# Kernel optimization log

Measured on AMD Instinct MI355X. Metric: run time of the kernel, lower is better.

The kernel has to match this reference:

```python
import jax, jax.numpy as jnp
import numpy as np

B, N, DIN, DOUT, L = 32, 512, 768, 256, 512
NEG = -9.0e15
SLOPE = 0.2  # LeakyReLU negative slope


def setup_inputs() -> dict:
    key = jax.random.key(0)
    ks = jax.random.split(key, 7)
    h = jax.random.normal(ks[0], (B, N, DIN), dtype=jnp.float32)
    adj = jax.random.randint(ks[1], (B, N, N), 0, 2, dtype=jnp.int32)
    positions = jax.random.randint(ks[2], (B, N), 0, L, dtype=jnp.int32)
    W = jax.random.normal(ks[3], (DIN, DOUT), dtype=jnp.float32) * 0.02
    a1 = jax.random.normal(ks[4], (DOUT,), dtype=jnp.float32) * 0.02
    a2 = jax.random.normal(ks[5], (DOUT,), dtype=jnp.float32) * 0.02
    pos_table = jax.random.normal(ks[6], (L, DOUT), dtype=jnp.float32) * 0.02
    return {"h": h, "adj": adj, "positions": positions, "W": W,
            "a1": a1, "a2": a2, "pos_table": pos_table}


def reference(h, adj, positions, W, a1, a2, pos_table):
    # Wh = W(h) + pos_emb(positions)   -> [B, N, DOUT]
    Wh = jnp.einsum('bnd,de->bne', h, W) + pos_table[positions]
    # Pairwise GAT score: e_ij = leakyrelu(a1 . Wh_i + a2 . Wh_j)
    # (identical math to concat([Wh_i, Wh_j]) @ [a1; a2], without the O(N^2*2D) tensor)
    s1 = jnp.einsum('bnd,d->bn', Wh, a1)  # source term   [B, N]
    s2 = jnp.einsum('bnd,d->bn', Wh, a2)  # target term   [B, N]
    e = jax.nn.leaky_relu(s1[:, :, None] + s2[:, None, :], negative_slope=SLOPE)  # [B,N,N]
    # adjacency mask + softmax over neighbors (dropout is identity in eval)
    attention = jax.nn.softmax(jnp.where(adj > 0, e, NEG), axis=-1)  # [B, N, N]
    h_prime = jnp.einsum('bij,bjd->bid', attention, Wh)  # [B, N, DOUT]
    return h_prime, attention
```

## Files before the change

### kernel.cpp

```cpp
#include <hip/hip_runtime.h>
#include <math.h>

#define B 32
#define N 512
#define DIN 768
#define DOUT 256
#define NEGV -9.0e15f
#define SLOPE 0.2f

typedef __bf16 bf16x8 __attribute__((ext_vector_type(8)));
typedef float f32x4 __attribute__((ext_vector_type(4)));
typedef unsigned short us8 __attribute__((ext_vector_type(8)));

__device__ __forceinline__ unsigned short f2b(float f) {
    union { float f; unsigned u; } v; v.f = f;
    unsigned r = v.u + 0x7FFF + ((v.u >> 16) & 1);
    return (unsigned short)(r >> 16);
}

__device__ __forceinline__ float b2f(unsigned short h) {
    union { unsigned u; float f; } v; v.u = ((unsigned)h) << 16;
    return v.f;
}

__device__ __forceinline__ void gload_lds16(const unsigned short* g, unsigned short* l) {
    __builtin_amdgcn_global_load_lds(
        (const __attribute__((address_space(1))) unsigned int*)(unsigned long long)(uintptr_t)g,
        (__attribute__((address_space(3))) unsigned int*)(uintptr_t)l,
        16, 0, 0);
}

__global__ __launch_bounds__(256) void conv_h(const float4* __restrict__ in,
                                              ushort4* __restrict__ out) {
    int idx = blockIdx.x * 256 + threadIdx.x;
    float4 v = in[idx];
    ushort4 o;
    o.x = f2b(v.x); o.y = f2b(v.y); o.z = f2b(v.z); o.w = f2b(v.w);
    out[idx] = o;
}

__global__ __launch_bounds__(256) void conv_wt(const float* __restrict__ W,
                                               unsigned short* __restrict__ WT) {
    __shared__ unsigned short tile[64][65];
    const int k0 = blockIdx.x * 64, n0 = blockIdx.y * 64;
    const int t = threadIdx.x;
    const int cl = t & 63, cg = t >> 6;
#pragma unroll
    for (int i = 0; i < 16; ++i) {
        int k = cg * 16 + i;
        tile[cl][k] = f2b(W[(size_t)(k0 + k) * DOUT + n0 + cl]);
    }
    __syncthreads();
#pragma unroll
    for (int i = 0; i < 16; ++i) {
        int n = cg * 16 + i;
        WT[(size_t)(n0 + n) * DIN + k0 + cl] = tile[n][cl];
    }
}

__global__ __launch_bounds__(256) void wh_mfma(
    const unsigned short* __restrict__ hA,
    const unsigned short* __restrict__ WT,
    const int*   __restrict__ pos,
    const float* __restrict__ ptab,
    unsigned short* __restrict__ WhT)
{
    constexpr int K = DIN;
    __shared__ unsigned short As[128 * 32];
    __shared__ unsigned short Bs[64 * 32];
    __shared__ unsigned short tileT[64 * 136];

    const int t    = threadIdx.x;
    const int lane = t & 63;
    const int w    = t >> 6;
    const int m0   = blockIdx.y * 128;
    const int n0   = blockIdx.x * 64;

    const int ar0 = t >> 2,          aq0 = (t & 3) ^ ((ar0 >> 1) & 3);
    const int ar1 = (256 + t) >> 2,  aq1 = (t & 3) ^ ((ar1 >> 1) & 3);
    const int br  = t >> 2,          bq  = (t & 3) ^ ((br >> 1) & 3);
    const unsigned short* gA0 = hA + (size_t)(m0 + ar0) * K + aq0 * 8;
    const unsigned short* gA1 = hA + (size_t)(m0 + ar1) * K + aq1 * 8;
    const unsigned short* gB  = WT + (size_t)(n0 + br) * K + bq * 8;
    unsigned short* lA0 = As + (t & 192) * 8;
    unsigned short* lA1 = As + 2048 + (t & 192) * 8;
    unsigned short* lB  = Bs + (t & 192) * 8;

    const int wm = (w & 1) * 64, wn = (w >> 1) * 32;
    const int l15 = lane & 15, q = lane >> 4;
    int aoff[4], boff[2];
#pragma unroll
    for (int i = 0; i < 4; ++i) {
        int rm = wm + i * 16 + l15;
        aoff[i] = (rm * 4 + (q ^ ((rm >> 1) & 3))) * 8;
    }
#pragma unroll
    for (int i = 0; i < 2; ++i) {
        int rn = wn + i * 16 + l15;
        boff[i] = (rn * 4 + (q ^ ((rn >> 1) & 3))) * 8;
    }

    f32x4 acc[4][2];
#pragma unroll
    for (int i = 0; i < 4; ++i)
#pragma unroll
        for (int j = 0; j < 2; ++j) acc[i][j] = (f32x4){0.f, 0.f, 0.f, 0.f};

    for (int k0 = 0; k0 < K; k0 += 32) {
        gload_lds16(gA0 + k0, lA0);
        gload_lds16(gA1 + k0, lA1);
        gload_lds16(gB + k0, lB);
        __syncthreads();
        bf16x8 af[4], bfr[2];
#pragma unroll
        for (int i = 0; i < 4; ++i) af[i] = *(const bf16x8*)(As + aoff[i]);
#pragma unroll
        for (int i = 0; i < 2; ++i) bfr[i] = *(const bf16x8*)(Bs + boff[i]);
#pragma unroll
        for (int mi = 0; mi < 4; ++mi)
#pragma unroll
            for (int ni = 0; ni < 2; ++ni)
                acc[mi][ni] = __builtin_amdgcn_mfma_f32_16x16x32_bf16(
                    af[mi], bfr[ni], acc[mi][ni], 0, 0, 0);
        __syncthreads();
    }

#pragma unroll
    for (int mi = 0; mi < 4; ++mi) {
        const int jb = wm + mi * 16 + q * 4;
#pragma unroll
        for (int ni = 0; ni < 2; ++ni) {
            const int nl = wn + ni * 16 + l15;
            ushort4 pk;
            unsigned short* pp = (unsigned short*)&pk;
#pragma unroll
            for (int r = 0; r < 4; ++r) {
                int m = m0 + jb + r;
                int p = pos[m];
                pp[r] = f2b(acc[mi][ni][r] + ptab[(size_t)p * DOUT + n0 + nl]);
            }
            *(ushort4*)&tileT[nl * 136 + jb] = pk;
        }
    }
    __syncthreads();
    const int bb = m0 >> 9, j0 = m0 & 511;
#pragma unroll
    for (int rr = 0; rr < 4; ++rr) {
        int nl = (t >> 4) + rr * 16;
        int jl = (t & 15) * 8;
        us8 v = *(const us8*)&tileT[nl * 136 + jl];
        *(us8*)&WhT[((size_t)bb * DOUT + n0 + nl) * N + j0 + jl] = v;
    }
}

__global__ __launch_bounds__(256) void rowdots(
    const unsigned short* __restrict__ WhT,
    const float* __restrict__ a1, const float* __restrict__ a2,
    float* __restrict__ s1, float* __restrict__ s2)
{
    const int b = blockIdx.x >> 3, jc = blockIdx.x & 7;
    const int jl = threadIdx.x & 63, dq = threadIdx.x >> 6;
    const int j = jc * 64 + jl;
    const unsigned short* base = WhT + (size_t)b * DOUT * N + j;
    float v1 = 0.f, v2 = 0.f;
#pragma unroll 8
    for (int dd = 0; dd < 64; ++dd) {
        int d = dq * 64 + dd;
        float wv = b2f(base[(size_t)d * N]);
        v1 += wv * a1[d];
        v2 += wv * a2[d];
    }
    __shared__ float r1[4][64], r2[4][64];
    r1[dq][jl] = v1; r2[dq][jl] = v2;
    __syncthreads();
    if (dq == 0) {
        s1[b * N + j] = r1[0][jl] + r1[1][jl] + r1[2][jl] + r1[3][jl];
        s2[b * N + j] = r2[0][jl] + r2[1][jl] + r2[2][jl] + r2[3][jl];
    }
}

__global__ __launch_bounds__(256) void attn_softmax(
    const float* __restrict__ s1,
    const float* __restrict__ s2,
    const int*   __restrict__ adj,
    float*       __restrict__ att,
    unsigned short* __restrict__ attb)
{
    const int row = blockIdx.x;
    const int b   = row >> 9;
    const int t   = threadIdx.x;

    const float s1i = s1[row];
    float vals[2];
#pragma unroll
    for (int c = 0; c < 2; ++c) {
        int j = t + c * 256;
        float v = s1i + s2[b * N + j];
        v = v > 0.0f ? v : SLOPE * v;
        vals[c] = (adj[(size_t)row * N + j] > 0) ? v : NEGV;
    }

    __shared__ float red[4];
    __shared__ float bcast;

    float m = fmaxf(vals[0], vals[1]);
#pragma unroll
    for (int off = 32; off > 0; off >>= 1)
        m = fmaxf(m, __shfl_down(m, off));
    const int wid = t >> 6;
    if ((t & 63) == 0) red[wid] = m;
    __syncthreads();
    if (t == 0) bcast = fmaxf(fmaxf(red[0], red[1]), fmaxf(red[2], red[3]));
    __syncthreads();
    m = bcast;

    float p0 = __expf(vals[0] - m);
    float p1 = __expf(vals[1] - m);
    float s = p0 + p1;
#pragma unroll
    for (int off = 32; off > 0; off >>= 1)
        s += __shfl_down(s, off);
    __syncthreads();
    if ((t & 63) == 0) red[wid] = s;
    __syncthreads();
    if (t == 0) bcast = red[0] + red[1] + red[2] + red[3];
    __syncthreads();
    const float inv = 1.0f / bcast;

    float o0 = p0 * inv, o1 = p1 * inv;
    att[(size_t)row * N + t]        = o0;
    att[(size_t)row * N + t + 256]  = o1;
    attb[(size_t)row * N + t]       = f2b(o0);
    attb[(size_t)row * N + t + 256] = f2b(o1);
}

__global__ __launch_bounds__(256) void hp_mfma(
    const unsigned short* __restrict__ attb,
    const unsigned short* __restrict__ WhT,
    float* __restrict__ hp)
{
    constexpr int K = N;
    __shared__ unsigned short As[128 * 32];
    __shared__ unsigned short Bs[64 * 32];

    const int t    = threadIdx.x;
    const int lane = t & 63;
    const int w    = t >> 6;
    const int bb   = blockIdx.z;
    const int m0   = blockIdx.y * 128;
    const int n0   = blockIdx.x * 64;

    const unsigned short* A  = attb + (size_t)bb * N * N;
    const unsigned short* Bg = WhT  + (size_t)bb * DOUT * N;

    const int ar0 = t >> 2,          aq0 = (t & 3) ^ ((ar0 >> 1) & 3);
    const int ar1 = (256 + t) >> 2,  aq1 = (t & 3) ^ ((ar1 >> 1) & 3);
    const int br  = t >> 2,          bq  = (t & 3) ^ ((br >> 1) & 3);
    const unsigned short* gA0 = A  + (size_t)(m0 + ar0) * K + aq0 * 8;
    const unsigned short* gA1 = A  + (size_t)(m0 + ar1) * K + aq1 * 8;
    const unsigned short* gB  = Bg + (size_t)(n0 + br) * K + bq * 8;
    unsigned short* lA0 = As + (t & 192) * 8;
    unsigned short* lA1 = As + 2048 + (t & 192) * 8;
    unsigned short* lB  = Bs + (t & 192) * 8;

    const int wm = (w & 1) * 64, wn = (w >> 1) * 32;
    const int l15 = lane & 15, q = lane >> 4;
    int aoff[4], boff[2];
#pragma unroll
    for (int i = 0; i < 4; ++i) {
        int rm = wm + i * 16 + l15;
        aoff[i] = (rm * 4 + (q ^ ((rm >> 1) & 3))) * 8;
    }
#pragma unroll
    for (int i = 0; i < 2; ++i) {
        int rn = wn + i * 16 + l15;
        boff[i] = (rn * 4 + (q ^ ((rn >> 1) & 3))) * 8;
    }

    f32x4 acc[4][2];
#pragma unroll
    for (int i = 0; i < 4; ++i)
#pragma unroll
        for (int j = 0; j < 2; ++j) acc[i][j] = (f32x4){0.f, 0.f, 0.f, 0.f};

    for (int k0 = 0; k0 < K; k0 += 32) {
        gload_lds16(gA0 + k0, lA0);
        gload_lds16(gA1 + k0, lA1);
        gload_lds16(gB + k0, lB);
        __syncthreads();
        bf16x8 af[4], bfr[2];
#pragma unroll
        for (int i = 0; i < 4; ++i) af[i] = *(const bf16x8*)(As + aoff[i]);
#pragma unroll
        for (int i = 0; i < 2; ++i) bfr[i] = *(const bf16x8*)(Bs + boff[i]);
#pragma unroll
        for (int mi = 0; mi < 4; ++mi)
#pragma unroll
            for (int ni = 0; ni < 2; ++ni)
                acc[mi][ni] = __builtin_amdgcn_mfma_f32_16x16x32_bf16(
                    af[mi], bfr[ni], acc[mi][ni], 0, 0, 0);
        __syncthreads();
    }

#pragma unroll
    for (int mi = 0; mi < 4; ++mi) {
#pragma unroll
        for (int r = 0; r < 4; ++r) {
            int m = m0 + wm + mi * 16 + q * 4 + r;
#pragma unroll
            for (int ni = 0; ni < 2; ++ni) {
                int n = n0 + wn + ni * 16 + l15;
                hp[((size_t)bb * N + m) * DOUT + n] = acc[mi][ni][r];
            }
        }
    }
}

extern "C" void kernel_launch(void* const* d_in, const int* in_sizes, int n_in,
                              void* d_out, int out_size, void* d_ws, size_t ws_size,
                              hipStream_t stream) {
    const float* h         = (const float*)d_in[0];
    const int*   adj       = (const int*)  d_in[1];
    const int*   positions = (const int*)  d_in[2];
    const float* W         = (const float*)d_in[3];
    const float* a1        = (const float*)d_in[4];
    const float* a2        = (const float*)d_in[5];
    const float* pos_table = (const float*)d_in[6];

    float* out     = (float*)d_out;
    float* h_prime = out;
    float* att     = out + (size_t)B * N * DOUT;

    char* ws = (char*)d_ws;
    unsigned short* h_bf  = (unsigned short*)ws;
    unsigned short* attb  = (unsigned short*)ws;
    unsigned short* WT    = (unsigned short*)(ws + 25165824);
    unsigned short* WhT   = (unsigned short*)(ws + 25559040);
    float*          s1    = (float*)(ws + 33947648);
    float*          s2    = s1 + (size_t)B * N;

    conv_h<<<(B * N * DIN) / 1024, 256, 0, stream>>>((const float4*)h, (ushort4*)h_bf);
    {
        dim3 grid(DIN / 64, DOUT / 64);
        conv_wt<<<grid, 256, 0, stream>>>(W, WT);
    }
    {
        dim3 grid(DOUT / 64, (B * N) / 128);
        wh_mfma<<<grid, 256, 0, stream>>>(h_bf, WT, positions, pos_table, WhT);
    }
    rowdots<<<B * 8, 256, 0, stream>>>(WhT, a1, a2, s1, s2);
    attn_softmax<<<B * N, 256, 0, stream>>>(s1, s2, adj, att, attb);
    {
        dim3 grid(DOUT / 64, N / 128, B);
        hp_mfma<<<grid, 256, 0, stream>>>(attb, WhT, h_prime);
    }
}
```

Measured before the change: 183.0 us.

## Fuse conversions, fold rowdots into Wh GEMM epilogue, deepen K tile

Merges the h and W conversion kernels into one launch. It drops the separate rowdots kernel by computing s1/s2 in the Wh GEMM epilogue with shuffle reductions and atomics into a zeroed buffer. Both MFMA GEMMs now use a 64-wide K step with an 8-way XOR swizzle and a linearised grid order that keeps blocks sharing an operand adjacent. The softmax kernel uses vectorised loads and stores. Together these cut launches and global passes, at the cost of an extra memset, atomic contention and a different order of float accumulation.

```diff
diff --git a/kernel.cpp b/kernel.cpp
--- a/kernel.cpp
+++ b/kernel.cpp
@@ -30,31 +30,32 @@
         16, 0, 0);
 }
 
-__global__ __launch_bounds__(256) void conv_h(const float4* __restrict__ in,
-                                              ushort4* __restrict__ out) {
-    int idx = blockIdx.x * 256 + threadIdx.x;
-    float4 v = in[idx];
-    ushort4 o;
-    o.x = f2b(v.x); o.y = f2b(v.y); o.z = f2b(v.z); o.w = f2b(v.w);
-    out[idx] = o;
-}
-
-__global__ __launch_bounds__(256) void conv_wt(const float* __restrict__ W,
-                                               unsigned short* __restrict__ WT) {
+__global__ __launch_bounds__(256) void conv_fused(
+    const float4* __restrict__ hin, ushort4* __restrict__ hout,
+    const float* __restrict__ W, unsigned short* __restrict__ WT) {
     __shared__ unsigned short tile[64][65];
-    const int k0 = blockIdx.x * 64, n0 = blockIdx.y * 64;
     const int t = threadIdx.x;
-    const int cl = t & 63, cg = t >> 6;
-#pragma unroll
-    for (int i = 0; i < 16; ++i) {
-        int k = cg * 16 + i;
-        tile[cl][k] = f2b(W[(size_t)(k0 + k) * DOUT + n0 + cl]);
-    }
-    __syncthreads();
-#pragma unroll
-    for (int i = 0; i < 16; ++i) {
-        int n = cg * 16 + i;
-        WT[(size_t)(n0 + n) * DIN + k0 + cl] = tile[n][cl];
+    if (blockIdx.x < 12288) {
+        int idx = blockIdx.x * 256 + t;
+        float4 v = hin[idx];
+        ushort4 o;
+        o.x = f2b(v.x); o.y = f2b(v.y); o.z = f2b(v.z); o.w = f2b(v.w);
+        hout[idx] = o;
+    } else {
+        int bid = blockIdx.x - 12288;
+        int k0 = (bid % 12) * 64, n0 = (bid / 12) * 64;
+        const int cl = t & 63, cg = t >> 6;
+#pragma unroll
+        for (int i = 0; i < 16; ++i) {
+            int k = cg * 16 + i;
+            tile[cl][k] = f2b(W[(size_t)(k0 + k) * DOUT + n0 + cl]);
+        }
+        __syncthreads();
+#pragma unroll
+        for (int i = 0; i < 16; ++i) {
+            int n = cg * 16 + i;
+            WT[(size_t)(n0 + n) * DIN + k0 + cl] = tile[n][cl];
+        }
     }
 }
 
@@ -63,41 +64,67 @@
     const unsigned short* __restrict__ WT,
     const int*   __restrict__ pos,
     const float* __restrict__ ptab,
-    unsigned short* __restrict__ WhT)
+    const float* __restrict__ a1,
+    const float* __restrict__ a2,
+    unsigned short* __restrict__ WhT,
+    float* __restrict__ s1, float* __restrict__ s2)
 {
     constexpr int K = DIN;
-    __shared__ unsigned short As[128 * 32];
-    __shared__ unsigned short Bs[64 * 32];
-    __shared__ unsigned short tileT[64 * 136];
+    __shared__ unsigned short smem[12288];
+    unsigned short* As = smem;
+    unsigned short* Bs = smem + 8192;
+    unsigned short* tileT = smem;
 
     const int t    = threadIdx.x;
     const int lane = t & 63;
     const int w    = t >> 6;
-    const int m0   = blockIdx.y * 128;
-    const int n0   = blockIdx.x * 64;
-
-    const int ar0 = t >> 2,          aq0 = (t & 3) ^ ((ar0 >> 1) & 3);
-    const int ar1 = (256 + t) >> 2,  aq1 = (t & 3) ^ ((ar1 >> 1) & 3);
-    const int br  = t >> 2,          bq  = (t & 3) ^ ((br >> 1) & 3);
-    const unsigned short* gA0 = hA + (size_t)(m0 + ar0) * K + aq0 * 8;
-    const unsigned short* gA1 = hA + (size_t)(m0 + ar1) * K + aq1 * 8;
-    const unsigned short* gB  = WT + (size_t)(n0 + br) * K + bq * 8;
-    unsigned short* lA0 = As + (t & 192) * 8;
-    unsigned short* lA1 = As + 2048 + (t & 192) * 8;
-    unsigned short* lB  = Bs + (t & 192) * 8;
+    const int lin  = blockIdx.x;
+    const int m0   = (lin & 127) * 128;
+    const int n0   = (lin >> 7) * 64;
+
+    int arow[4], apos[4];
+#pragma unroll
+    for (int i = 0; i < 4; ++i) {
+        int c = i * 256 + t;
+        arow[i] = c >> 3;
+        apos[i] = (c & 7) ^ ((c >> 3) & 7);
+    }
+    int brow[2], bpos[2];
+#pragma unroll
+    for (int i = 0; i < 2; ++i) {
+        int c = i * 256 + t;
+        brow[i] = c >> 3;
+        bpos[i] = (c & 7) ^ ((c >> 3) & 7);
+    }
+    const unsigned short* gA[4];
+    const unsigned short* gB[2];
+#pragma unroll
+    for (int i = 0; i < 4; ++i) gA[i] = hA + (size_t)(m0 + arow[i]) * K + apos[i] * 8;
+#pragma unroll
+    for (int i = 0; i < 2; ++i) gB[i] = WT + (size_t)(n0 + brow[i]) * K + bpos[i] * 8;
+    unsigned short* lA[4];
+    unsigned short* lB[2];
+#pragma unroll
+    for (int i = 0; i < 4; ++i) lA[i] = As + (i * 256 + (t & 192)) * 8;
+#pragma unroll
+    for (int i = 0; i < 2; ++i) lB[i] = Bs + (i * 256 + (t & 192)) * 8;
 
     const int wm = (w & 1) * 64, wn = (w >> 1) * 32;
     const int l15 = lane & 15, q = lane >> 4;
-    int aoff[4], boff[2];
-#pragma unroll
-    for (int i = 0; i < 4; ++i) {
-        int rm = wm + i * 16 + l15;
-        aoff[i] = (rm * 4 + (q ^ ((rm >> 1) & 3))) * 8;
-    }
-#pragma unroll
-    for (int i = 0; i < 2; ++i) {
-        int rn = wn + i * 16 + l15;
-        boff[i] = (rn * 4 + (q ^ ((rn >> 1) & 3))) * 8;
+    int aoff[2][4], boff[2][2];
+#pragma unroll
+    for (int kk = 0; kk < 2; ++kk) {
+        int pg = kk * 4 + q;
+#pragma unroll
+        for (int i = 0; i < 4; ++i) {
+            int rm = wm + i * 16 + l15;
+            aoff[kk][i] = rm * 64 + ((pg ^ (rm & 7)) * 8);
+        }
+#pragma unroll
+        for (int i = 0; i < 2; ++i) {
+            int rn = wn + i * 16 + l15;
+            boff[kk][i] = rn * 64 + ((pg ^ (rn & 7)) * 8);
+        }
     }
 
     f32x4 acc[4][2];
@@ -106,28 +133,35 @@
 #pragma unroll
         for (int j = 0; j < 2; ++j) acc[i][j] = (f32x4){0.f, 0.f, 0.f, 0.f};
 
-    for (int k0 = 0; k0 < K; k0 += 32) {
-        gload_lds16(gA0 + k0, lA0);
-        gload_lds16(gA1 + k0, lA1);
-        gload_lds16(gB + k0, lB);
-        __syncthreads();
-        bf16x8 af[4], bfr[2];
-#pragma unroll
-        for (int i = 0; i < 4; ++i) af[i] = *(const bf16x8*)(As + aoff[i]);
-#pragma unroll
-        for (int i = 0; i < 2; ++i) bfr[i] = *(const bf16x8*)(Bs + boff[i]);
-#pragma unroll
-        for (int mi = 0; mi < 4; ++mi)
-#pragma unroll
-            for (int ni = 0; ni < 2; ++ni)
-                acc[mi][ni] = __builtin_amdgcn_mfma_f32_16x16x32_bf16(
-                    af[mi], bfr[ni], acc[mi][ni], 0, 0, 0);
-        __syncthreads();
-    }
-
+    for (int k0 = 0; k0 < K; k0 += 64) {
+#pragma unroll
+        for (int i = 0; i < 4; ++i) gload_lds16(gA[i] + k0, lA[i]);
+#pragma unroll
+        for (int i = 0; i < 2; ++i) gload_lds16(gB[i] + k0, lB[i]);
+        __syncthreads();
+#pragma unroll
+        for (int kk = 0; kk < 2; ++kk) {
+            bf16x8 af[4], bfr[2];
+#pragma unroll
+            for (int i = 0; i < 4; ++i) af[i] = *(const bf16x8*)(As + aoff[kk][i]);
+#pragma unroll
+            for (int i = 0; i < 2; ++i) bfr[i] = *(const bf16x8*)(Bs + boff[kk][i]);
+#pragma unroll
+            for (int mi = 0; mi < 4; ++mi)
+#pragma unroll
+                for (int ni = 0; ni < 2; ++ni)
+                    acc[mi][ni] = __builtin_amdgcn_mfma_f32_16x16x32_bf16(
+                        af[mi], bfr[ni], acc[mi][ni], 0, 0, 0);
+        }
+        __syncthreads();
+    }
+
+    const float a1v[2] = { a1[n0 + wn + l15], a1[n0 + wn + 16 + l15] };
+    const float a2v[2] = { a2[n0 + wn + l15], a2[n0 + wn + 16 + l15] };
 #pragma unroll
     for (int mi = 0; mi < 4; ++mi) {
         const int jb = wm + mi * 16 + q * 4;
+        float v[2][4];
 #pragma unroll
         for (int ni = 0; ni < 2; ++ni) {
             const int nl = wn + ni * 16 + l15;
@@ -137,9 +171,25 @@
             for (int r = 0; r < 4; ++r) {
                 int m = m0 + jb + r;
                 int p = pos[m];
-                pp[r] = f2b(acc[mi][ni][r] + ptab[(size_t)p * DOUT + n0 + nl]);
+                float val = acc[mi][ni][r] + ptab[(size_t)p * DOUT + n0 + nl];
+                v[ni][r] = val;
+                pp[r] = f2b(val);
             }
             *(ushort4*)&tileT[nl * 136 + jb] = pk;
+        }
+#pragma unroll
+        for (int r = 0; r < 4; ++r) {
+            float t1 = v[0][r] * a1v[0] + v[1][r] * a1v[1];
+            float t2 = v[0][r] * a2v[0] + v[1][r] * a2v[1];
+#pragma unroll
+            for (int mk = 1; mk < 16; mk <<= 1) {
+                t1 += __shfl_xor(t1, mk);
+                t2 += __shfl_xor(t2, mk);
+            }
+            if (l15 == 0) {
+                atomicAdd(&s1[m0 + jb + r], t1);
+                atomicAdd(&s2[m0 + jb + r], t2);
+            }
         }
     }
     __syncthreads();
@@ -148,34 +198,8 @@
     for (int rr = 0; rr < 4; ++rr) {
         int nl = (t >> 4) + rr * 16;
         int jl = (t & 15) * 8;
-        us8 v = *(const us8*)&tileT[nl * 136 + jl];
-        *(us8*)&WhT[((size_t)bb * DOUT + n0 + nl) * N + j0 + jl] = v;
-    }
-}
-
-__global__ __launch_bounds__(256) void rowdots(
-    const unsigned short* __restrict__ WhT,
-    const float* __restrict__ a1, const float* __restrict__ a2,
-    float* __restrict__ s1, float* __restrict__ s2)
-{
-    const int b = blockIdx.x >> 3, jc = blockIdx.x & 7;
-    const int jl = threadIdx.x & 63, dq = threadIdx.x >> 6;
-    const int j = jc * 64 + jl;
-    const unsigned short* base = WhT + (size_t)b * DOUT * N + j;
-    float v1 = 0.f, v2 = 0.f;
-#pragma unroll 8
-    for (int dd = 0; dd < 64; ++dd) {
-        int d = dq * 64 + dd;
-        float wv = b2f(base[(size_t)d * N]);
-        v1 += wv * a1[d];
-        v2 += wv * a2[d];
-    }
-    __shared__ float r1[4][64], r2[4][64];
-    r1[dq][jl] = v1; r2[dq][jl] = v2;
-    __syncthreads();
-    if (dq == 0) {
-        s1[b * N + j] = r1[0][jl] + r1[1][jl] + r1[2][jl] + r1[3][jl];
-        s2[b * N + j] = r2[0][jl] + r2[1][jl] + r2[2][jl] + r2[3][jl];
+        us8 vv = *(const us8*)&tileT[nl * 136 + jl];
+        *(us8*)&WhT[((size_t)bb * DOUT + n0 + nl) * N + j0 + jl] = vv;
     }
 }
 
@@ -184,26 +208,25 @@
     const float* __restrict__ s2,
     const int*   __restrict__ adj,
     float*       __restrict__ att,
-    unsigned short* __restrict__ attb)
+    unsigned int* __restrict__ attb)
 {
     const int row = blockIdx.x;
     const int b   = row >> 9;
     const int t   = threadIdx.x;
 
     const float s1i = s1[row];
-    float vals[2];
-#pragma unroll
-    for (int c = 0; c < 2; ++c) {
-        int j = t + c * 256;
-        float v = s1i + s2[b * N + j];
-        v = v > 0.0f ? v : SLOPE * v;
-        vals[c] = (adj[(size_t)row * N + j] > 0) ? v : NEGV;
-    }
+    const float2 s2p = ((const float2*)(s2 + b * N))[t];
+    const int2   ap  = ((const int2*)(adj + (size_t)row * N))[t];
+
+    float v0 = s1i + s2p.x; v0 = v0 > 0.f ? v0 : SLOPE * v0;
+    float v1 = s1i + s2p.y; v1 = v1 > 0.f ? v1 : SLOPE * v1;
+    v0 = (ap.x > 0) ? v0 : NEGV;
+    v1 = (ap.y > 0) ? v1 : NEGV;
 
     __shared__ float red[4];
     __shared__ float bcast;
 
-    float m = fmaxf(vals[0], vals[1]);
+    float m = fmaxf(v0, v1);
 #pragma unroll
     for (int off = 32; off > 0; off >>= 1)
         m = fmaxf(m, __shfl_down(m, off));
@@ -214,8 +237,8 @@
     __syncthreads();
     m = bcast;
 
-    float p0 = __expf(vals[0] - m);
-    float p1 = __expf(vals[1] - m);
+    float p0 = __expf(v0 - m);
+    float p1 = __expf(v1 - m);
     float s = p0 + p1;
 #pragma unroll
     for (int off = 32; off > 0; off >>= 1)
@@ -228,10 +251,8 @@
     const float inv = 1.0f / bcast;
 
     float o0 = p0 * inv, o1 = p1 * inv;
-    att[(size_t)row * N + t]        = o0;
-    att[(size_t)row * N + t + 256]  = o1;
-    attb[(size_t)row * N + t]       = f2b(o0);
-    attb[(size_t)row * N + t + 256] = f2b(o1);
+    ((float2*)(att + (size_t)row * N))[t] = (float2){o0, o1};
+    attb[(size_t)row * 256 + t] = (unsigned)f2b(o0) | ((unsigned)f2b(o1) << 16);
 }
 
 __global__ __launch_bounds__(256) void hp_mfma(
@@ -240,41 +261,65 @@
     float* __restrict__ hp)
 {
     constexpr int K = N;
-    __shared__ unsigned short As[128 * 32];
-    __shared__ unsigned short Bs[64 * 32];
+    __shared__ unsigned short smem[12288];
+    unsigned short* As = smem;
+    unsigned short* Bs = smem + 8192;
 
     const int t    = threadIdx.x;
     const int lane = t & 63;
     const int w    = t >> 6;
-    const int bb   = blockIdx.z;
-    const int m0   = blockIdx.y * 128;
-    const int n0   = blockIdx.x * 64;
+    const int lin  = blockIdx.x;
+    const int n0   = (lin >> 7) * 64;
+    const int rest = lin & 127;
+    const int bb   = rest >> 2;
+    const int m0   = (rest & 3) * 128;
 
     const unsigned short* A  = attb + (size_t)bb * N * N;
     const unsigned short* Bg = WhT  + (size_t)bb * DOUT * N;
 
-    const int ar0 = t >> 2,          aq0 = (t & 3) ^ ((ar0 >> 1) & 3);
-    const int ar1 = (256 + t) >> 2,  aq1 = (t & 3) ^ ((ar1 >> 1) & 3);
-    const int br  = t >> 2,          bq  = (t & 3) ^ ((br >> 1) & 3);
-    const unsigned short* gA0 = A  + (size_t)(m0 + ar0) * K + aq0 * 8;
-    const unsigned short* gA1 = A  + (size_t)(m0 + ar1) * K + aq1 * 8;
-    const unsigned short* gB  = Bg + (size_t)(n0 + br) * K + bq * 8;
-    unsigned short* lA0 = As + (t & 192) * 8;
-    unsigned short* lA1 = As + 2048 + (t & 192) * 8;
-    unsigned short* lB  = Bs + (t & 192) * 8;
+    int arow[4], apos[4];
+#pragma unroll
+    for (int i = 0; i < 4; ++i) {
+        int c = i * 256 + t;
+        arow[i] = c >> 3;
+        apos[i] = (c & 7) ^ ((c >> 3) & 7);
+    }
+    int brow[2], bpos[2];
+#pragma unroll
+    for (int i = 0; i < 2; ++i) {
+        int c = i * 256 + t;
+        brow[i] = c >> 3;
+        bpos[i] = (c & 7) ^ ((c >> 3) & 7);
+    }
+    const unsigned short* gA[4];
+    const unsigned short* gB[2];
+#pragma unroll
+    for (int i = 0; i < 4; ++i) gA[i] = A + (size_t)(m0 + arow[i]) * K + apos[i] * 8;
+#pragma unroll
+    for (int i = 0; i < 2; ++i) gB[i] = Bg + (size_t)(n0 + brow[i]) * K + bpos[i] * 8;
+    unsigned short* lA[4];
+    unsigned short* lB[2];
+#pragma unroll
+    for (int i = 0; i < 4; ++i) lA[i] = As + (i * 256 + (t & 192)) * 8;
+#pragma unroll
+    for (int i = 0; i < 2; ++i) lB[i] = Bs + (i * 256 + (t & 192)) * 8;
 
     const int wm = (w & 1) * 64, wn = (w >> 1) * 32;
     const int l15 = lane & 15, q = lane >> 4;
-    int aoff[4], boff[2];
-#pragma unroll
-    for (int i = 0; i < 4; ++i) {
-        int rm = wm + i * 16 + l15;
-        aoff[i] = (rm * 4 + (q ^ ((rm >> 1) & 3))) * 8;
-    }
-#pragma unroll
-    for (int i = 0; i < 2; ++i) {
-        int rn = wn + i * 16 + l15;
-        boff[i] = (rn * 4 + (q ^ ((rn >> 1) & 3))) * 8;
+    int aoff[2][4], boff[2][2];
+#pragma unroll
+    for (int kk = 0; kk < 2; ++kk) {
+        int pg = kk * 4 + q;
+#pragma unroll
+        for (int i = 0; i < 4; ++i) {
+            int rm = wm + i * 16 + l15;
+            aoff[kk][i] = rm * 64 + ((pg ^ (rm & 7)) * 8);
+        }
+#pragma unroll
+        for (int i = 0; i < 2; ++i) {
+            int rn = wn + i * 16 + l15;
+            boff[kk][i] = rn * 64 + ((pg ^ (rn & 7)) * 8);
+        }
     }
 
     f32x4 acc[4][2];
@@ -283,22 +328,26 @@
 #pragma unroll
         for (int j = 0; j < 2; ++j) acc[i][j] = (f32x4){0.f, 0.f, 0.f, 0.f};
 
-    for (int k0 = 0; k0 < K; k0 += 32) {
-        gload_lds16(gA0 + k0, lA0);
-        gload_lds16(gA1 + k0, lA1);
-        gload_lds16(gB + k0, lB);
-        __syncthreads();
-        bf16x8 af[4], bfr[2];
-#pragma unroll
-        for (int i = 0; i < 4; ++i) af[i] = *(const bf16x8*)(As + aoff[i]);
-#pragma unroll
-        for (int i = 0; i < 2; ++i) bfr[i] = *(const bf16x8*)(Bs + boff[i]);
-#pragma unroll
-        for (int mi = 0; mi < 4; ++mi)
-#pragma unroll
-            for (int ni = 0; ni < 2; ++ni)
-                acc[mi][ni] = __builtin_amdgcn_mfma_f32_16x16x32_bf16(
-                    af[mi], bfr[ni], acc[mi][ni], 0, 0, 0);
+    for (int k0 = 0; k0 < K; k0 += 64) {
+#pragma unroll
+        for (int i = 0; i < 4; ++i) gload_lds16(gA[i] + k0, lA[i]);
+#pragma unroll
+        for (int i = 0; i < 2; ++i) gload_lds16(gB[i] + k0, lB[i]);
+        __syncthreads();
+#pragma unroll
+        for (int kk = 0; kk < 2; ++kk) {
+            bf16x8 af[4], bfr[2];
+#pragma unroll
+            for (int i = 0; i < 4; ++i) af[i] = *(const bf16x8*)(As + aoff[kk][i]);
+#pragma unroll
+            for (int i = 0; i < 2; ++i) bfr[i] = *(const bf16x8*)(Bs + boff[kk][i]);
+#pragma unroll
+            for (int mi = 0; mi < 4; ++mi)
+#pragma unroll
+                for (int ni = 0; ni < 2; ++ni)
+                    acc[mi][ni] = __builtin_amdgcn_mfma_f32_16x16x32_bf16(
+                        af[mi], bfr[ni], acc[mi][ni], 0, 0, 0);
+        }
         __syncthreads();
     }
 
@@ -339,19 +388,9 @@
     float*          s1    = (float*)(ws + 33947648);
     float*          s2    = s1 + (size_t)B * N;
 
-    conv_h<<<(B * N * DIN) / 1024, 256, 0, stream>>>((const float4*)h, (ushort4*)h_bf);
-    {
-        dim3 grid(DIN / 64, DOUT / 64);
-        conv_wt<<<grid, 256, 0, stream>>>(W, WT);
-    }
-    {
-        dim3 grid(DOUT / 64, (B * N) / 128);
-        wh_mfma<<<grid, 256, 0, stream>>>(h_bf, WT, positions, pos_table, WhT);
-    }
-    rowdots<<<B * 8, 256, 0, stream>>>(WhT, a1, a2, s1, s2);
-    attn_softmax<<<B * N, 256, 0, stream>>>(s1, s2, adj, att, attb);
-    {
-        dim3 grid(DOUT / 64, N / 128, B);
-        hp_mfma<<<grid, 256, 0, stream>>>(attb, WhT, h_prime);
-    }
-}
+    hipMemsetAsync(s1, 0, (size_t)2 * B * N * sizeof(float), stream);
+    conv_fused<<<12288 + 48, 256, 0, stream>>>((const float4*)h, (ushort4*)h_bf, W, WT);
+    wh_mfma<<<512, 256, 0, stream>>>(h_bf, WT, positions, pos_table, a1, a2, WhT, s1, s2);
+    attn_softmax<<<B * N, 256, 0, stream>>>(s1, s2, adj, att, (unsigned int*)attb);
+    hp_mfma<<<512, 256, 0, stream>>>(attb, WhT, h_prime);
+}
```

After: 172.0 us. -6.0%, faster.
